# Kernel tuning notes

Hardware: AMD Instinct MI355X
Metric: run time of the kernel (lower is better)

Reference implementation:

```python
import jax, jax.numpy as jnp
import numpy as np
from jax import lax

SCORE_THRESHOLD = 0.5
IOU_THRESHOLD = 0.5
IMG_SIZE = 640.0
SPLITTER_THRESHOLD = 0.0
N = 4096


def setup_inputs() -> dict:
    key = jax.random.key(0)
    # raw RT-DETR output: [1, N, 5] = (cx, cy, w, h, person_conf), all in [0, 1]
    rtdetr_raw_out = jax.random.uniform(key, (1, N, 5), dtype=jnp.float32)
    return {"rtdetr_raw_out": rtdetr_raw_out}


def _iou_matrix(boxes):
    # boxes: [N, 4] in xyxy. Returns [N, N] pairwise IoU.
    x1, y1, x2, y2 = boxes[:, 0], boxes[:, 1], boxes[:, 2], boxes[:, 3]
    area = (x2 - x1) * (y2 - y1)  # [N]
    ix1 = jnp.maximum(x1[:, None], x1[None, :])
    iy1 = jnp.maximum(y1[:, None], y1[None, :])
    ix2 = jnp.minimum(x2[:, None], x2[None, :])
    iy2 = jnp.minimum(y2[:, None], y2[None, :])
    iw = jnp.clip(ix2 - ix1, 0.0)
    ih = jnp.clip(iy2 - iy1, 0.0)
    inter = iw * ih
    union = area[:, None] + area[None, :] - inter
    return inter / jnp.maximum(union, 1e-9)


def reference(rtdetr_raw_out):
    raw = rtdetr_raw_out[0]  # squeeze(0) -> [N, 5]
    conf = raw[:, 4]
    # splitter: keep boxes with conf > 0.0 (expressed as a mask for fixed shapes)
    valid = conf > SPLITTER_THRESHOLD
    # cxcywh scaled to pixel coords, then converted to xyxy
    cxcywh = raw[:, :4] * IMG_SIZE
    cx, cy, w, h = cxcywh[:, 0], cxcywh[:, 1], cxcywh[:, 2], cxcywh[:, 3]
    xyxy = jnp.stack([cx - w * 0.5, cy - h * 0.5, cx + w * 0.5, cy + h * 0.5], axis=1)
    # NMS score filter: conf >= score_threshold
    valid = valid & (conf >= SCORE_THRESHOLD)
    # sort by score descending; invalid boxes sink to the bottom with -inf keys
    sort_key = jnp.where(valid, conf, -jnp.inf)
    order = jnp.argsort(-sort_key)
    boxes_s = xyxy[order]          # [N, 4]
    conf_s = conf[order]           # [N]
    valid_s = valid[order]         # [N]
    iou = _iou_matrix(boxes_s)     # [N, N]
    idx = jnp.arange(N)

    def body(i, keep):
        keep_i = keep[i]
        # suppress any lower-ranked box with IoU > threshold to a kept box i
        sup = (iou[i] > IOU_THRESHOLD) & keep_i & (idx > i)
        return keep & (~sup)

    keep = lax.fori_loop(0, N, body, valid_s)
    boxes_and_scores = jnp.concatenate([boxes_s, conf_s[:, None]], axis=1)  # [N, 5]
    # fixed-shape equivalent of boolean-gather: suppressed/invalid rows zeroed
    return boxes_and_scores * keep[:, None].astype(boxes_and_scores.dtype)
```

## Files before the change

kernel.cpp:

```cpp
#include <hip/hip_runtime.h>
#include <stdint.h>

#define NBOX 4096
#define IMG 640.0f

typedef unsigned long long u64;
typedef unsigned int u32;


__global__ __launch_bounds__(256) void k_rank(const float* __restrict__ raw,
                                              int* __restrict__ rank_partial, int* __restrict__ Mp) {
    const int bi = blockIdx.x, bj = blockIdx.y;
    const int t = threadIdx.x;
    const int i = bi * 256 + t;
    if (bi == 0 && bj == 0 && t == 0) *Mp = 0;
    __shared__ float cj[256];
    cj[t] = raw[(bj * 256 + t) * 5 + 4];
    __syncthreads();

    const float ci = raw[i * 5 + 4];
    const int jbase = bj * 256;
    int rank = 0;
    const float4* c4 = reinterpret_cast<const float4*>(cj);
#pragma unroll 4
    for (int j4 = 0; j4 < 64; ++j4) {
        float4 c = c4[j4];
        int j = jbase + j4 * 4;
        rank += (c.x > ci || (c.x == ci && (j + 0) < i)) ? 1 : 0;
        rank += (c.y > ci || (c.y == ci && (j + 1) < i)) ? 1 : 0;
        rank += (c.z > ci || (c.z == ci && (j + 2) < i)) ? 1 : 0;
        rank += (c.w > ci || (c.w == ci && (j + 3) < i)) ? 1 : 0;
    }
    rank_partial[bj * NBOX + i] = rank;
}

__global__ __launch_bounds__(256) void k_scatter(const float* __restrict__ raw,
                                                 const int* __restrict__ rank_partial,
                                                 float* __restrict__ sx1, float* __restrict__ sy1,
                                                 float* __restrict__ sx2, float* __restrict__ sy2,
                                                 float* __restrict__ sconf, int* __restrict__ Mp) {
    const int i = blockIdx.x * 256 + threadIdx.x;
    const float ci = raw[i * 5 + 4];
    const bool vi = (ci >= 0.5f);

    int rank = 0;
#pragma unroll
    for (int k = 0; k < 16; ++k) rank += rank_partial[k * NBOX + i];

    u64 bal = __ballot(vi);
    if ((threadIdx.x & 63) == 0) atomicAdd(Mp, (int)__popcll(bal));

    if (vi) {
        float cx = __fmul_rn(raw[i * 5 + 0], IMG);
        float cy = __fmul_rn(raw[i * 5 + 1], IMG);
        float w  = __fmul_rn(raw[i * 5 + 2], IMG);
        float h  = __fmul_rn(raw[i * 5 + 3], IMG);
        float hw = __fmul_rn(w, 0.5f);
        float hh = __fmul_rn(h, 0.5f);
        sx1[rank]   = __fsub_rn(cx, hw);
        sy1[rank]   = __fsub_rn(cy, hh);
        sx2[rank]   = __fadd_rn(cx, hw);
        sy2[rank]   = __fadd_rn(cy, hh);
        sconf[rank] = ci;
    }
}

__global__ __launch_bounds__(256) void k_mask(const float* __restrict__ sx1, const float* __restrict__ sy1,
                                              const float* __restrict__ sx2, const float* __restrict__ sy2,
                                              const int* __restrict__ Mp,
                                              u64* __restrict__ maskT, u64* __restrict__ diagR,
                                              u64* __restrict__ carry1) {
    const int w = blockIdx.y;
    const int r = blockIdx.x * 256 + threadIdx.x;
    const int t = threadIdx.x;
    const int M = *Mp;

    __shared__ float cx1[64], cy1[64], cx2[64], cy2[64], car[64];
    if (t < 64) {
        int j = (w << 6) + t;
        float a1 = sx1[j], b1 = sy1[j], a2 = sx2[j], b2 = sy2[j];
        cx1[t] = a1; cy1[t] = b1; cx2[t] = a2; cy2[t] = b2;
        car[t] = __fmul_rn(__fsub_rn(a2, a1), __fsub_rn(b2, b1));
    }
    __syncthreads();

    u64 bits = 0ULL;
    if (r < M) {
        const float x1 = sx1[r], y1 = sy1[r], x2 = sx2[r], y2 = sy2[r];
        const float area_i = __fmul_rn(__fsub_rn(x2, x1), __fsub_rn(y2, y1));
        const int bmax = min(64, M - (w << 6));
        const int bmin = max(0, r + 1 - (w << 6));
        for (int b = bmin; b < bmax; ++b) {
            float xx1 = fmaxf(x1, cx1[b]);
            float yy1 = fmaxf(y1, cy1[b]);
            float xx2 = fminf(x2, cx2[b]);
            float yy2 = fminf(y2, cy2[b]);
            float iw = fmaxf(__fsub_rn(xx2, xx1), 0.0f);
            float ih = fmaxf(__fsub_rn(yy2, yy1), 0.0f);
            float inter = __fmul_rn(iw, ih);
            float uni = __fsub_rn(__fadd_rn(area_i, car[b]), inter);
            float iou = __fdiv_rn(inter, fmaxf(uni, 1e-9f));
            if (iou > 0.5f) bits |= (1ULL << b);
        }
        maskT[((size_t)w << 12) + r] = bits;
    }

    const int rblk = r >> 6;
    if (rblk == w)     diagR[r]  = bits;
    if (rblk + 1 == w) carry1[r] = bits;
}

__global__ __launch_bounds__(576) void k_scan(const int* __restrict__ Mp,
                                              const u64* __restrict__ maskT,
                                              const u64* __restrict__ diagR,
                                              const u64* __restrict__ carry1,
                                              const float* __restrict__ sx1, const float* __restrict__ sy1,
                                              const float* __restrict__ sx2, const float* __restrict__ sy2,
                                              const float* __restrict__ sconf,
                                              float* __restrict__ out) {
    __shared__ u64 remvArr[64];
    __shared__ u64 kbArr[64];
    const int tid = threadIdx.x;
    const int wave = tid >> 6;
    const int lane = tid & 63;
    const int M = *Mp;
    const int nblk = (M + 63) >> 6;

    if (tid < 64) { remvArr[tid] = 0ULL; kbArr[tid] = 0ULL; }
    __syncthreads();

    if (nblk > 0) {
        if (wave == 0) {
            __builtin_amdgcn_s_setprio(1);
            u64 d0 = 0, d1 = 0, d2 = 0, d3 = 0, d4 = 0, d5 = 0;
            u64 e0 = 0, e1 = 0, e2 = 0, e3 = 0, e4 = 0, e5 = 0;
            d0 = diagR[lane];                 e0 = carry1[lane];
            if (1 < nblk) { d1 = diagR[(1 << 6) + lane]; e1 = carry1[(1 << 6) + lane]; }
            if (2 < nblk) { d2 = diagR[(2 << 6) + lane]; e2 = carry1[(2 << 6) + lane]; }
            if (3 < nblk) { d3 = diagR[(3 << 6) + lane]; e3 = carry1[(3 << 6) + lane]; }
            if (4 < nblk) { d4 = diagR[(4 << 6) + lane]; e4 = carry1[(4 << 6) + lane]; }
            if (5 < nblk) { d5 = diagR[(5 << 6) + lane]; e5 = carry1[(5 << 6) + lane]; }
            u64 carry = 0ULL;

#define W0STEP(B, DD, EE)                                                     \
    do {                                                                      \
        const int b_ = (B);                                                   \
        if (b_ < nblk) {                                                      \
            const u64 rb = remvArr[b_] | carry;                               \
            const int rem = M - (b_ << 6);                                    \
            const u64 valid = (rem >= 64) ? ~0ULL : ((1ULL << rem) - 1ULL);   \
            u64 alive = valid & ~rb;                                          \
            u64 kb = 0ULL, car = 0ULL;                                        \
            const u32 dlo = (u32)(DD), dhi = (u32)((DD) >> 32);               \
            const u32 el = (u32)(EE), eh = (u32)((EE) >> 32);                 \
            while (alive) {                                                   \
                int i = __builtin_ctzll(alive); alive &= alive - 1;           \
                kb |= (1ULL << i);                                            \
                u32 lo = (u32)__builtin_amdgcn_readlane(dlo, i);              \
                u32 hi = (u32)__builtin_amdgcn_readlane(dhi, i);              \
                u32 p  = (u32)__builtin_amdgcn_readlane(el, i);               \
                u32 q  = (u32)__builtin_amdgcn_readlane(eh, i);               \
                alive &= ~(((u64)hi << 32) | (u64)lo);          \
                car |= ((u64)q << 32) | (u64)p;                \
            }                                                                 \
            carry = car;                                                      \
            if (lane == 0) kbArr[b_] = kb;                                    \
            if (b_ + 6 < nblk) {                                              \
                (DD) = diagR [((b_ + 6) << 6) + lane];                        \
                (EE) = carry1[((b_ + 6) << 6) + lane];                        \
            }                                                                 \
            asm volatile("s_waitcnt lgkmcnt(0)" ::: "memory");                \
            __builtin_amdgcn_s_barrier();                                     \
            __builtin_amdgcn_sched_barrier(0);                                \
        }                                                                     \
    } while (0)

            for (int base = 0; base < nblk; base += 6) {
                W0STEP(base + 0, d0, e0);
                W0STEP(base + 1, d1, e1);
                W0STEP(base + 2, d2, e2);
                W0STEP(base + 3, d3, e3);
                W0STEP(base + 4, d4, e4);
                W0STEP(base + 5, d5, e5);
            }
#undef W0STEP
        } else {
            const int w1 = wave - 1;
            const int chunk = tid & 7;
            const int slot = (tid >> 3) & 7;
            u64 vA[8], vB[8], vC[8];

#define BISSUE(V, T)                                                           \
    do {                                                                       \
        const int W_ = (T) + 1 + (w1 << 3) + slot;                             \
        const int Wc_ = (W_ < 64) ? W_ : 63;                                   \
        const u64* cb_ = maskT + ((size_t)Wc_ << 12) + ((size_t)((T) - 1) << 6); \
        _Pragma("unroll")                                                      \
        for (int k = 0; k < 8; ++k) (V)[k] = cb_[chunk + (k << 3)];            \
    } while (0)

#define BFOLD(V, T)                                                            \
    do {                                                                       \
        const u64 kb_ = kbArr[(T) - 1];                                        \
        const int W_ = (T) + 1 + (w1 << 3) + slot;                             \
        if (W_ < 64 && kb_ != 0ULL) {                                          \
            u64 acc_ = 0ULL;                                                   \
            _Pragma("unroll")                                                  \
            for (int k = 0; k < 8; ++k)                                        \
                acc_ |= (((kb_ >> (chunk + (k << 3))) & 1ULL) ? (V)[k] : 0ULL); \
            acc_ |= __shfl_xor(acc_, 1);                                       \
            acc_ |= __shfl_xor(acc_, 2);                                       \
            acc_ |= __shfl_xor(acc_, 4);                                       \
            if (chunk == 0) remvArr[W_] |= acc_;                               \
        }                                                                      \
    } while (0)

#define BSTEP(T, V)                                                            \
    do {                                                                       \
        const int t_ = (T);                                                    \
        if (t_ < nblk) {                                                       \
            if (t_ >= 1) BFOLD(V, t_);                                         \
            if (t_ + 3 < nblk) BISSUE(V, t_ + 3);                              \
            asm volatile("s_waitcnt lgkmcnt(0)" ::: "memory");                 \
            __builtin_amdgcn_s_barrier();                                      \
            __builtin_amdgcn_sched_barrier(0);                                 \
        }                                                                      \
    } while (0)

            if (1 < nblk) BISSUE(vB, 1);
            if (2 < nblk) BISSUE(vC, 2);
            for (int base = 0; base < nblk; base += 3) {
                BSTEP(base + 0, vA);
                BSTEP(base + 1, vB);
                BSTEP(base + 2, vC);
            }
#undef BISSUE
#undef BFOLD
#undef BSTEP
        }
    }
    __syncthreads();

    for (int g = tid; g < NBOX * 5; g += 576) {
        const int r = g / 5;
        const int c = g - r * 5;
        bool kept = false;
        if (r < M) kept = ((kbArr[r >> 6] >> (r & 63)) & 1ULL) != 0ULL;
        float vv = 0.0f;
        if (kept) {
            const float* arr = (c == 0) ? sx1 : (c == 1) ? sy1 : (c == 2) ? sx2 : (c == 3) ? sy2 : sconf;
            vv = arr[r];
        }
        out[g] = vv;
    }
}

extern "C" void kernel_launch(void* const* d_in, const int* in_sizes, int n_in,
                              void* d_out, int out_size, void* d_ws, size_t ws_size,
                              hipStream_t stream) {
    const float* raw = (const float*)d_in[0];
    char* ws = (char*)d_ws;
    float* sx1 = (float*)(ws + 0);
    float* sy1 = (float*)(ws + 16384);
    float* sx2 = (float*)(ws + 32768);
    float* sy2 = (float*)(ws + 49152);
    float* sconf = (float*)(ws + 65536);
    int* Mp = (int*)(ws + 81920);
    u64* diagR  = (u64*)(ws + 86016);
    u64* carry1 = (u64*)(ws + 118784);
    u64* maskT = (u64*)(ws + 196608);
    int* rank_partial = (int*)(ws + 2293760);
    float* out = (float*)d_out;

    k_rank<<<dim3(16, 16), dim3(256), 0, stream>>>(raw, rank_partial, Mp);
    k_scatter<<<dim3(16), dim3(256), 0, stream>>>(raw, rank_partial, sx1, sy1, sx2, sy2, sconf, Mp);
    k_mask<<<dim3(16, 64), dim3(256), 0, stream>>>(sx1, sy1, sx2, sy2, Mp, maskT, diagR, carry1);
    k_scan<<<dim3(1), dim3(576), 0, stream>>>(Mp, maskT, diagR, carry1, sx1, sy1, sx2, sy2, sconf, out);
}
```

Baseline: 87.63 us.

## Fold suppression rows in the scan wave instead of helper waves with barriers

Stores the IoU mask row-major so each kept box's suppression row can be gathered with one coalesced load per lane. The scan wave now issues up to 16 row loads per kept block itself, double-buffered across alternating register sets, ORs them into a per-lane removal word, and reads the next block's removed bits with readlane. This removes the 8 helper waves, the shared-memory remvArr and the per-block workgroup barriers. In exchange it puts the global-load latency on the serial critical path and adds a slow fallback loop for blocks that keep more than 16 boxes.

```diff
diff --git a/kernel.cpp b/kernel.cpp
--- a/kernel.cpp
+++ b/kernel.cpp
@@ -68,7 +68,7 @@
 __global__ __launch_bounds__(256) void k_mask(const float* __restrict__ sx1, const float* __restrict__ sy1,
                                               const float* __restrict__ sx2, const float* __restrict__ sy2,
                                               const int* __restrict__ Mp,
-                                              u64* __restrict__ maskT, u64* __restrict__ diagR,
+                                              u64* __restrict__ mask, u64* __restrict__ diagR,
                                               u64* __restrict__ carry1) {
     const int w = blockIdx.y;
     const int r = blockIdx.x * 256 + threadIdx.x;
@@ -102,7 +102,7 @@
             float iou = __fdiv_rn(inter, fmaxf(uni, 1e-9f));
             if (iou > 0.5f) bits |= (1ULL << b);
         }
-        maskT[((size_t)w << 12) + r] = bits;
+        mask[((size_t)r << 6) + w] = bits;
     }
 
     const int rblk = r >> 6;
@@ -110,43 +110,89 @@
     if (rblk + 1 == w) carry1[r] = bits;
 }
 
-__global__ __launch_bounds__(576) void k_scan(const int* __restrict__ Mp,
-                                              const u64* __restrict__ maskT,
+__global__ __launch_bounds__(256) void k_scan(const int* __restrict__ Mp,
+                                              const u64* __restrict__ mask,
                                               const u64* __restrict__ diagR,
                                               const u64* __restrict__ carry1,
                                               const float* __restrict__ sx1, const float* __restrict__ sy1,
                                               const float* __restrict__ sx2, const float* __restrict__ sy2,
                                               const float* __restrict__ sconf,
                                               float* __restrict__ out) {
-    __shared__ u64 remvArr[64];
     __shared__ u64 kbArr[64];
     const int tid = threadIdx.x;
-    const int wave = tid >> 6;
     const int lane = tid & 63;
     const int M = *Mp;
     const int nblk = (M + 63) >> 6;
 
-    if (tid < 64) { remvArr[tid] = 0ULL; kbArr[tid] = 0ULL; }
-    __syncthreads();
-
-    if (nblk > 0) {
-        if (wave == 0) {
-            __builtin_amdgcn_s_setprio(1);
-            u64 d0 = 0, d1 = 0, d2 = 0, d3 = 0, d4 = 0, d5 = 0;
-            u64 e0 = 0, e1 = 0, e2 = 0, e3 = 0, e4 = 0, e5 = 0;
-            d0 = diagR[lane];                 e0 = carry1[lane];
-            if (1 < nblk) { d1 = diagR[(1 << 6) + lane]; e1 = carry1[(1 << 6) + lane]; }
-            if (2 < nblk) { d2 = diagR[(2 << 6) + lane]; e2 = carry1[(2 << 6) + lane]; }
-            if (3 < nblk) { d3 = diagR[(3 << 6) + lane]; e3 = carry1[(3 << 6) + lane]; }
-            if (4 < nblk) { d4 = diagR[(4 << 6) + lane]; e4 = carry1[(4 << 6) + lane]; }
-            if (5 < nblk) { d5 = diagR[(5 << 6) + lane]; e5 = carry1[(5 << 6) + lane]; }
-            u64 carry = 0ULL;
-
-#define W0STEP(B, DD, EE)                                                     \
+    if (tid < 64) kbArr[tid] = 0ULL;
+
+    if ((tid >> 6) == 0 && nblk > 0) {
+        __builtin_amdgcn_s_setprio(1);
+
+        u64 d0 = 0, d1 = 0, d2 = 0, d3 = 0, d4 = 0, d5 = 0;
+        u64 e0 = 0, e1 = 0, e2 = 0, e3 = 0, e4 = 0, e5 = 0;
+        d0 = diagR[lane];                 e0 = carry1[lane];
+        if (1 < nblk) { d1 = diagR[(1 << 6) + lane]; e1 = carry1[(1 << 6) + lane]; }
+        if (2 < nblk) { d2 = diagR[(2 << 6) + lane]; e2 = carry1[(2 << 6) + lane]; }
+        if (3 < nblk) { d3 = diagR[(3 << 6) + lane]; e3 = carry1[(3 << 6) + lane]; }
+        if (4 < nblk) { d4 = diagR[(4 << 6) + lane]; e4 = carry1[(4 << 6) + lane]; }
+        if (5 < nblk) { d5 = diagR[(5 << 6) + lane]; e5 = carry1[(5 << 6) + lane]; }
+
+        u64 fA0=0,fA1=0,fA2=0,fA3=0,fA4=0,fA5=0,fA6=0,fA7=0,
+            fA8=0,fA9=0,fA10=0,fA11=0,fA12=0,fA13=0,fA14=0,fA15=0;
+        u64 fB0=0,fB1=0,fB2=0,fB3=0,fB4=0,fB5=0,fB6=0,fB7=0,
+            fB8=0,fB9=0,fB10=0,fB11=0,fB12=0,fB13=0,fB14=0,fB15=0;
+        int cntA = 0, cntB = 0;
+        u64 ofA = 0ULL, ofB = 0ULL;
+
+        u32 rvlo = 0, rvhi = 0;
+        u64 carry = 0ULL;
+
+#define FOLD16(P, BF)                                                         \
+    do {                                                                      \
+        if (cnt##P) {                                                         \
+            u64 facc = f##P##0 | f##P##1 | f##P##2 | f##P##3                  \
+                     | f##P##4 | f##P##5 | f##P##6 | f##P##7                  \
+                     | f##P##8 | f##P##9 | f##P##10 | f##P##11                \
+                     | f##P##12 | f##P##13 | f##P##14 | f##P##15;             \
+            if (__builtin_expect(of##P != 0ULL, 0)) {                         \
+                u64 tt_ = of##P;                                              \
+                const u64* rb2_ = mask + ((size_t)(((BF) - 2) << 6) << 6);    \
+                while (tt_) { int ii_ = __builtin_ctzll(tt_); tt_ &= tt_ - 1; \
+                              facc |= rb2_[((size_t)ii_ << 6) + lane]; }      \
+            }                                                                 \
+            rvlo |= (u32)facc; rvhi |= (u32)(facc >> 32);                     \
+        }                                                                     \
+    } while (0)
+
+#define ISLOT(NAME)                                                           \
+    do {                                                                      \
+        const int ik_ = tt_ ? __builtin_ctzll(tt_) : i0_;                     \
+        if (tt_) tt_ &= tt_ - 1;                                              \
+        NAME = rowb_[((size_t)ik_ << 6) + lane];                              \
+    } while (0)
+
+#define ISSUE16(P, BI)                                                        \
+    do {                                                                      \
+        u64 tt_ = kb;                                                         \
+        const int i0_ = kb ? __builtin_ctzll(kb) : 0;                         \
+        const u64* rowb_ = mask + ((size_t)((BI) << 6) << 6);                 \
+        ISLOT(f##P##0);  ISLOT(f##P##1);  ISLOT(f##P##2);  ISLOT(f##P##3);    \
+        ISLOT(f##P##4);  ISLOT(f##P##5);  ISLOT(f##P##6);  ISLOT(f##P##7);    \
+        ISLOT(f##P##8);  ISLOT(f##P##9);  ISLOT(f##P##10); ISLOT(f##P##11);   \
+        ISLOT(f##P##12); ISLOT(f##P##13); ISLOT(f##P##14); ISLOT(f##P##15);   \
+        cnt##P = (kb != 0ULL) ? 1 : 0;                                        \
+        of##P = tt_;                                                          \
+    } while (0)
+
+#define STEP(B, DD, EE, P)                                                    \
     do {                                                                      \
         const int b_ = (B);                                                   \
         if (b_ < nblk) {                                                      \
-            const u64 rb = remvArr[b_] | carry;                               \
+            FOLD16(P, b_);                        \
+            u32 rbl = (u32)__builtin_amdgcn_readlane(rvlo, b_);               \
+            u32 rbh = (u32)__builtin_amdgcn_readlane(rvhi, b_);               \
+            const u64 rb = (((u64)rbh << 32) | (u64)rbl) | carry;             \
             const int rem = M - (b_ << 6);                                    \
             const u64 valid = (rem >= 64) ? ~0ULL : ((1ULL << rem) - 1ULL);   \
             u64 alive = valid & ~rb;                                          \
@@ -165,83 +211,30 @@
             }                                                                 \
             carry = car;                                                      \
             if (lane == 0) kbArr[b_] = kb;                                    \
+            ISSUE16(P, b_);                                \
             if (b_ + 6 < nblk) {                                              \
                 (DD) = diagR [((b_ + 6) << 6) + lane];                        \
                 (EE) = carry1[((b_ + 6) << 6) + lane];                        \
             }                                                                 \
-            asm volatile("s_waitcnt lgkmcnt(0)" ::: "memory");                \
-            __builtin_amdgcn_s_barrier();                                     \
-            __builtin_amdgcn_sched_barrier(0);                                \
         }                                                                     \
     } while (0)
 
-            for (int base = 0; base < nblk; base += 6) {
-                W0STEP(base + 0, d0, e0);
-                W0STEP(base + 1, d1, e1);
-                W0STEP(base + 2, d2, e2);
-                W0STEP(base + 3, d3, e3);
-                W0STEP(base + 4, d4, e4);
-                W0STEP(base + 5, d5, e5);
-            }
-#undef W0STEP
-        } else {
-            const int w1 = wave - 1;
-            const int chunk = tid & 7;
-            const int slot = (tid >> 3) & 7;
-            u64 vA[8], vB[8], vC[8];
-
-#define BISSUE(V, T)                                                           \
-    do {                                                                       \
-        const int W_ = (T) + 1 + (w1 << 3) + slot;                             \
-        const int Wc_ = (W_ < 64) ? W_ : 63;                                   \
-        const u64* cb_ = maskT + ((size_t)Wc_ << 12) + ((size_t)((T) - 1) << 6); \
-        _Pragma("unroll")                                                      \
-        for (int k = 0; k < 8; ++k) (V)[k] = cb_[chunk + (k << 3)];            \
-    } while (0)
-
-#define BFOLD(V, T)                                                            \
-    do {                                                                       \
-        const u64 kb_ = kbArr[(T) - 1];                                        \
-        const int W_ = (T) + 1 + (w1 << 3) + slot;                             \
-        if (W_ < 64 && kb_ != 0ULL) {                                          \
-            u64 acc_ = 0ULL;                                                   \
-            _Pragma("unroll")                                                  \
-            for (int k = 0; k < 8; ++k)                                        \
-                acc_ |= (((kb_ >> (chunk + (k << 3))) & 1ULL) ? (V)[k] : 0ULL); \
-            acc_ |= __shfl_xor(acc_, 1);                                       \
-            acc_ |= __shfl_xor(acc_, 2);                                       \
-            acc_ |= __shfl_xor(acc_, 4);                                       \
-            if (chunk == 0) remvArr[W_] |= acc_;                               \
-        }                                                                      \
-    } while (0)
-
-#define BSTEP(T, V)                                                            \
-    do {                                                                       \
-        const int t_ = (T);                                                    \
-        if (t_ < nblk) {                                                       \
-            if (t_ >= 1) BFOLD(V, t_);                                         \
-            if (t_ + 3 < nblk) BISSUE(V, t_ + 3);                              \
-            asm volatile("s_waitcnt lgkmcnt(0)" ::: "memory");                 \
-            __builtin_amdgcn_s_barrier();                                      \
-            __builtin_amdgcn_sched_barrier(0);                                 \
-        }                                                                      \
-    } while (0)
-
-            if (1 < nblk) BISSUE(vB, 1);
-            if (2 < nblk) BISSUE(vC, 2);
-            for (int base = 0; base < nblk; base += 3) {
-                BSTEP(base + 0, vA);
-                BSTEP(base + 1, vB);
-                BSTEP(base + 2, vC);
-            }
-#undef BISSUE
-#undef BFOLD
-#undef BSTEP
+        for (int base = 0; base < nblk; base += 6) {
+            STEP(base + 0, d0, e0, A);
+            STEP(base + 1, d1, e1, B);
+            STEP(base + 2, d2, e2, A);
+            STEP(base + 3, d3, e3, B);
+            STEP(base + 4, d4, e4, A);
+            STEP(base + 5, d5, e5, B);
         }
+#undef STEP
+#undef ISSUE16
+#undef ISLOT
+#undef FOLD16
     }
     __syncthreads();
 
-    for (int g = tid; g < NBOX * 5; g += 576) {
+    for (int g = tid; g < NBOX * 5; g += 256) {
         const int r = g / 5;
         const int c = g - r * 5;
         bool kept = false;
@@ -268,12 +261,12 @@
     int* Mp = (int*)(ws + 81920);
     u64* diagR  = (u64*)(ws + 86016);
     u64* carry1 = (u64*)(ws + 118784);
-    u64* maskT = (u64*)(ws + 196608);
+    u64* mask = (u64*)(ws + 196608);
     int* rank_partial = (int*)(ws + 2293760);
     float* out = (float*)d_out;
 
     k_rank<<<dim3(16, 16), dim3(256), 0, stream>>>(raw, rank_partial, Mp);
     k_scatter<<<dim3(16), dim3(256), 0, stream>>>(raw, rank_partial, sx1, sy1, sx2, sy2, sconf, Mp);
-    k_mask<<<dim3(16, 64), dim3(256), 0, stream>>>(sx1, sy1, sx2, sy2, Mp, maskT, diagR, carry1);
-    k_scan<<<dim3(1), dim3(576), 0, stream>>>(Mp, maskT, diagR, carry1, sx1, sy1, sx2, sy2, sconf, out);
-}
+    k_mask<<<dim3(16, 64), dim3(256), 0, stream>>>(sx1, sy1, sx2, sy2, Mp, mask, diagR, carry1);
+    k_scan<<<dim3(1), dim3(256), 0, stream>>>(Mp, mask, diagR, carry1, sx1, sy1, sx2, sy2, sconf, out);
+}
```

After: 152.8 us. 74.4% more time.
